# Kernel optimization log

Hardware: AMD Instinct MI355X
Metric: run time of the kernel (lower is better)

## Reference

```python
import jax, jax.numpy as jnp
import numpy as np

UNITS = 14336
IN_FEATURES = 4096
PACKED = IN_FEATURES // 4  # 4 ternary values (2 bits each) per byte
CLIP_VAL = 100.0

# 2-bit crumb -> ternary value lookup: 0 -> 0, 1 -> +1, 2 -> -1, 3 -> 0
_TERNARY_LUT = jnp.array([0.0, 1.0, -1.0, 0.0], dtype=jnp.float32)


def _unpack_ternary(pw):
    """pw: [U, P] int (byte values 0..255) -> dense ternary float W [U, 4*P].
    Little-endian crumbs within each byte (shifts 0,2,4,6)."""
    crumbs = jnp.stack([(pw >> (2 * i)) & 3 for i in range(4)], axis=-1)  # [U, P, 4]
    crumbs = crumbs.reshape(pw.shape[0], -1)  # [U, 4*P]
    return _TERNARY_LUT[crumbs][:, :IN_FEATURES]  # [U, IN]


def setup_inputs() -> dict:
    key = jax.random.key(0)
    k1, k2, k3, k4 = jax.random.split(key, 4)
    x = jax.random.normal(k1, (32, IN_FEATURES), dtype=jnp.float32)
    # packed ternary weights, one uint8-valued byte per 4 ternary weights
    pw = jax.random.randint(k2, (UNITS, PACKED), 0, 256, dtype=jnp.int32)
    scale = 1.0 + 0.02 * jax.random.normal(k3, (UNITS,), dtype=jnp.float32)
    bias = 0.01 * jax.random.normal(k4, (UNITS,), dtype=jnp.float32)
    return {"x": x, "pw": pw, "scale": scale, "bias": bias}


def reference(x, pw, scale, bias):
    # dense ternary weight [UNITS, IN]; kernel target would fuse this unpack into the GEMM
    W = _unpack_ternary(pw)
    y = jnp.einsum('bd,ud->bu', x, W)  # [B, UNITS]
    y = y * scale + bias               # per-unit affine dequant
    return jnp.clip(y, -CLIP_VAL, CLIP_VAL)
```

## Files before the change

kernel.cpp:

```cpp
#include <hip/hip_runtime.h>

#define UNITS 14336
#define IN_F 4096
#define PACKED 1024
#define CLIP_VAL 100.0f

typedef unsigned int uint32;

using bf16x8 = __attribute__((ext_vector_type(8))) short;
using f32x4  = __attribute__((ext_vector_type(4))) float;

__device__ inline unsigned short f2bf(float f) {
    uint32 u = __float_as_uint(f);
    u += 0x7FFFu + ((u >> 16) & 1u);
    return (unsigned short)(u >> 16);
}

__device__ inline uint32 pack2bf(float a, float b) {
    return (uint32)f2bf(a) | ((uint32)f2bf(b) << 16);
}

__device__ inline void unpack_byte(int v, uint32& r0, uint32& r1) {
    uint32 t0 = ((uint32)v & 3u) | (((uint32)v & 0xCu) << 14);
    uint32 t1 = (((uint32)v >> 4) & 3u) | (((uint32)v & 0xC0u) << 10);
    uint32 s0 = t0 >> 1;
    uint32 s1 = t1 >> 1;
    uint32 nz0 = (t0 ^ s0) & 0x00010001u;
    uint32 nz1 = (t1 ^ s1) & 0x00010001u;
    r0 = nz0 * 0x3F80u + ((s0 & 0x00010001u) << 15);
    r1 = nz1 * 0x3F80u + ((s1 & 0x00010001u) << 15);
}

__device__ inline float clipf(float y) {
    return fminf(fmaxf(y, -CLIP_VAL), CLIP_VAL);
}


__global__ __launch_bounds__(256) void convert_x_kernel(
    const float* __restrict__ x, uint4* __restrict__ ws) {
    int b = blockIdx.x;
    int c = b & 7;
    int t = ((b >> 3) << 8) + threadIdx.x;
    int lane = t & 63;
    int h = (t >> 6) & 1;
    int s = (t >> 7) & 1;
    int g = t >> 8;
    int n = lane & 15;
    int q = lane >> 4;
    int bi = h * 16 + n;
    int k0 = g * 64 + q * 16 + s * 8;
    const float4* src = (const float4*)(x + (size_t)bi * IN_F + k0);
    float4 lo = src[0];
    float4 hi = src[1];
    uint4 o;
    o.x = pack2bf(lo.x, lo.y);
    o.y = pack2bf(lo.z, lo.w);
    o.z = pack2bf(hi.x, hi.y);
    o.w = pack2bf(hi.z, hi.w);
    ws[c * 16384 + t] = o;
}

__global__ __launch_bounds__(1024, 8) void ternary_mm_kernel(
    const uint4* __restrict__ xw,
    const int*   __restrict__ pw,
    const float* __restrict__ scale,
    const float* __restrict__ bias,
    float*       __restrict__ out) {
    __shared__ int lds[16384];

    const int tid  = threadIdx.x;
    const int wid  = tid >> 6;
    const int lane = tid & 63;
    const int q    = lane >> 4;
    const int n    = lane & 15;
    const int u0   = blockIdx.x << 4;
    const int g0   = wid << 2;

    {
        const char* src = (const char*)(pw + (size_t)u0 * PACKED);
        #pragma unroll
        for (int r = 0; r < 4; ++r) {
            const int off = ((r * 16 + wid) << 10) + (lane << 4);
            __builtin_amdgcn_global_load_lds(
                (const __attribute__((address_space(1))) uint32*)(src + off),
                (__attribute__((address_space(3))) uint32*)((char*)lds + off),
                16, 0, 0);
        }
    }

    const uint4* xb = xw + ((blockIdx.x & 7) * 16384) + (g0 << 8) + lane;
    uint4 xa0 = xb[0], xa1 = xb[64], xa2 = xb[128], xa3 = xb[192];

    __syncthreads();

    f32x4 acc0 = {0.f,0.f,0.f,0.f};
    f32x4 acc1 = {0.f,0.f,0.f,0.f};
    const char* lb = (const char*)lds + (n << 12) + (q << 4);

    #pragma unroll
    for (int i = 0; i < 4; ++i) {
        uint4 xn0, xn1, xn2, xn3;
        if (i < 3) {
            const uint4* xi = xb + ((i + 1) << 8);
            xn0 = xi[0]; xn1 = xi[64]; xn2 = xi[128]; xn3 = xi[192];
        }
        int4 w4 = *(const int4*)(lb + ((g0 + i) << 6));

        uint4 fA, fB;
        unpack_byte(w4.x, fA.x, fA.y);
        unpack_byte(w4.y, fA.z, fA.w);
        unpack_byte(w4.z, fB.x, fB.y);
        unpack_byte(w4.w, fB.z, fB.w);
        bf16x8 vA = __builtin_bit_cast(bf16x8, fA);
        bf16x8 vB = __builtin_bit_cast(bf16x8, fB);

        acc0 = __builtin_amdgcn_mfma_f32_16x16x32_bf16(
            __builtin_bit_cast(bf16x8, xa0), vA, acc0, 0, 0, 0);
        acc1 = __builtin_amdgcn_mfma_f32_16x16x32_bf16(
            __builtin_bit_cast(bf16x8, xa1), vA, acc1, 0, 0, 0);
        acc0 = __builtin_amdgcn_mfma_f32_16x16x32_bf16(
            __builtin_bit_cast(bf16x8, xa2), vB, acc0, 0, 0, 0);
        acc1 = __builtin_amdgcn_mfma_f32_16x16x32_bf16(
            __builtin_bit_cast(bf16x8, xa3), vB, acc1, 0, 0, 0);

        if (i < 3) { xa0 = xn0; xa1 = xn1; xa2 = xn2; xa3 = xn3; }
    }

    __syncthreads();
    f32x4* red = (f32x4*)lds;
    red[(wid * 2 + 0) * 64 + lane] = acc0;
    red[(wid * 2 + 1) * 64 + lane] = acc1;
    __syncthreads();

    if (tid < 128) {
        const int h = tid >> 6;
        const int l = tid & 63;
        f32x4 s = red[h * 64 + l];
        #pragma unroll
        for (int w = 1; w < 16; ++w) {
            f32x4 v = red[(w * 2 + h) * 64 + l];
            s[0] += v[0]; s[1] += v[1]; s[2] += v[2]; s[3] += v[3];
        }
        const int u  = u0 + (l & 15);
        const int b0 = h * 16 + ((l >> 4) << 2);
        const float sc = scale[u];
        const float bi = bias[u];
        float* o = out + (size_t)b0 * UNITS + u;
        o[0 * UNITS] = clipf(s[0] * sc + bi);
        o[1 * UNITS] = clipf(s[1] * sc + bi);
        o[2 * UNITS] = clipf(s[2] * sc + bi);
        o[3 * UNITS] = clipf(s[3] * sc + bi);
    }
}

extern "C" void kernel_launch(void* const* d_in, const int* in_sizes, int n_in,
                              void* d_out, int out_size, void* d_ws, size_t ws_size,
                              hipStream_t stream) {
    const float* x     = (const float*)d_in[0];
    const int*   pw    = (const int*)d_in[1];
    const float* scale = (const float*)d_in[2];
    const float* bias  = (const float*)d_in[3];
    float* out = (float*)d_out;

    uint4* xw = (uint4*)d_ws;

    convert_x_kernel<<<512, 256, 0, stream>>>(x, xw);
    ternary_mm_kernel<<<UNITS / 16, 1024, 0, stream>>>(xw, pw, scale, bias, out);
}
```

Measured before the change: 104.5 us.

## Pad LDS weight rows to avoid bank conflicts and drop replicated x copies

Result: no change. 103.0 us (-1.3%).

```diff
diff --git a/kernel.cpp b/kernel.cpp
--- a/kernel.cpp
+++ b/kernel.cpp
@@ -38,18 +38,16 @@
 
 __global__ __launch_bounds__(256) void convert_x_kernel(
     const float* __restrict__ x, uint4* __restrict__ ws) {
-    int b = blockIdx.x;
-    int c = b & 7;
-    int t = ((b >> 3) << 8) + threadIdx.x;
+    int t = blockIdx.x * 256 + threadIdx.x;
     int lane = t & 63;
     int h = (t >> 6) & 1;
     int s = (t >> 7) & 1;
     int g = t >> 8;
     int n = lane & 15;
     int q = lane >> 4;
-    int bi = h * 16 + n;
+    int b = h * 16 + n;
     int k0 = g * 64 + q * 16 + s * 8;
-    const float4* src = (const float4*)(x + (size_t)bi * IN_F + k0);
+    const float4* src = (const float4*)(x + (size_t)b * IN_F + k0);
     float4 lo = src[0];
     float4 hi = src[1];
     uint4 o;
@@ -57,7 +55,7 @@
     o.y = pack2bf(lo.z, lo.w);
     o.z = pack2bf(hi.x, hi.y);
     o.w = pack2bf(hi.z, hi.w);
-    ws[c * 16384 + t] = o;
+    ws[t] = o;
 }
 
 __global__ __launch_bounds__(1024, 8) void ternary_mm_kernel(
@@ -66,7 +64,8 @@
     const float* __restrict__ scale,
     const float* __restrict__ bias,
     float*       __restrict__ out) {
-    __shared__ int lds[16384];
+    __shared__ int lds4[16640];
+    char* lds = (char*)lds4;
 
     const int tid  = threadIdx.x;
     const int wid  = tid >> 6;
@@ -79,23 +78,27 @@
     {
         const char* src = (const char*)(pw + (size_t)u0 * PACKED);
         #pragma unroll
-        for (int r = 0; r < 4; ++r) {
-            const int off = ((r * 16 + wid) << 10) + (lane << 4);
+        for (int j = 0; j < 4; ++j) {
+            const int Rs = j * 16 + wid;
             __builtin_amdgcn_global_load_lds(
-                (const __attribute__((address_space(1))) uint32*)(src + off),
-                (__attribute__((address_space(3))) uint32*)((char*)lds + off),
+                (const __attribute__((address_space(1))) uint32*)
+                    (src + (Rs << 10) + (lane << 4)),
+                (__attribute__((address_space(3))) uint32*)
+                    (lds + Rs * 1040),
                 16, 0, 0);
         }
     }
 
-    const uint4* xb = xw + ((blockIdx.x & 7) * 16384) + (g0 << 8) + lane;
+    const uint4* xb = xw + (g0 << 8) + lane;
     uint4 xa0 = xb[0], xa1 = xb[64], xa2 = xb[128], xa3 = xb[192];
 
     __syncthreads();
 
     f32x4 acc0 = {0.f,0.f,0.f,0.f};
     f32x4 acc1 = {0.f,0.f,0.f,0.f};
-    const char* lb = (const char*)lds + (n << 12) + (q << 4);
+
+    const int R = (n << 2) + (wid >> 2);
+    const char* lb = lds + R * 1040 + ((wid & 3) << 8) + (q << 4);
 
     #pragma unroll
     for (int i = 0; i < 4; ++i) {
@@ -104,7 +107,7 @@
             const uint4* xi = xb + ((i + 1) << 8);
             xn0 = xi[0]; xn1 = xi[64]; xn2 = xi[128]; xn3 = xi[192];
         }
-        int4 w4 = *(const int4*)(lb + ((g0 + i) << 6));
+        int4 w4 = *(const int4*)(lb + (i << 6));
 
         uint4 fA, fB;
         unpack_byte(w4.x, fA.x, fA.y);
@@ -164,6 +167,6 @@
 
     uint4* xw = (uint4*)d_ws;
 
-    convert_x_kernel<<<512, 256, 0, stream>>>(x, xw);
+    convert_x_kernel<<<64, 256, 0, stream>>>(x, xw);
     ternary_mm_kernel<<<UNITS / 16, 1024, 0, stream>>>(xw, pw, scale, bias, out);
 }
```
